# Kernel tuning notes

Measured on AMD Instinct MI355X. Metric: run time of the kernel, lower is better.

## Reference

```python
import jax, jax.numpy as jnp
import numpy as np

D_MODEL = 256
N_HEADS = 8
HEAD_DIM = D_MODEL // N_HEADS  # 32
N_LEVELS = 4
N_POINTS = 4
LEVEL_SHAPES = [(100, 100), (50, 50), (25, 25), (13, 13)]
LEVEL_STARTS = [0] + list(np.cumsum([h * w for h, w in LEVEL_SHAPES]))[:-1]
LEN_IN = int(sum(h * w for h, w in LEVEL_SHAPES))  # 13294
BATCH = 2
LEN_Q = LEN_IN  # encoder self-attention


def _offset_bias():
    # faithful to MSDeformAttn._reset_parameters for sampling_offsets bias
    thetas = np.arange(N_HEADS, dtype=np.float32) * (2.0 * np.pi / N_HEADS)
    grid = np.stack([np.cos(thetas), np.sin(thetas)], -1)
    grid = grid / np.abs(grid).max(-1, keepdims=True)
    grid = np.tile(grid.reshape(N_HEADS, 1, 1, 2), (1, N_LEVELS, N_POINTS, 1))
    for i in range(N_POINTS):
        grid[:, :, i, :] *= i + 1
    return jnp.asarray(grid.reshape(-1), dtype=jnp.float32)


def setup_inputs() -> dict:
    key = jax.random.key(0)
    ks = jax.random.split(key, 10)
    s = 1.0 / np.sqrt(D_MODEL)
    inp = {
        "query": jax.random.normal(ks[0], (BATCH, LEN_Q, D_MODEL), jnp.float32),
        "reference_points": jax.random.uniform(ks[1], (BATCH, LEN_Q, N_LEVELS, 2), jnp.float32),
        "input_flatten": jax.random.normal(ks[2], (BATCH, LEN_IN, D_MODEL), jnp.float32),
        "input_spatial_shapes": jnp.asarray(LEVEL_SHAPES, dtype=jnp.int32),
        "W_value": jax.random.normal(ks[3], (D_MODEL, D_MODEL), jnp.float32) * s,
        "b_value": jnp.zeros((D_MODEL,), jnp.float32),
        "W_off": jax.random.normal(ks[4], (D_MODEL, N_HEADS * N_LEVELS * N_POINTS * 2), jnp.float32) * 0.01,
        "b_off": _offset_bias(),
        "W_attn": jax.random.normal(ks[5], (D_MODEL, N_HEADS * N_LEVELS * N_POINTS), jnp.float32) * 0.01,
        "b_attn": jnp.zeros((N_HEADS * N_LEVELS * N_POINTS,), jnp.float32),
        "W_out": jax.random.normal(ks[6], (D_MODEL, D_MODEL), jnp.float32) * s,
        "b_out": jnp.zeros((D_MODEL,), jnp.float32),
    }
    return inp


def _corner(v_t, ix, iy, h, w):
    # v_t: (n, M, h*w, D); ix/iy: (n, M, LqP) int32. Zero padding outside.
    valid = (ix >= 0) & (ix < w) & (iy >= 0) & (iy < h)
    idx = jnp.clip(iy, 0, h - 1) * w + jnp.clip(ix, 0, w - 1)
    g = jnp.take_along_axis(v_t, idx[..., None], axis=2)  # (n, M, LqP, D)
    return g * valid[..., None].astype(v_t.dtype)


def _ms_deform_attn(query, reference_points, input_flatten,
                    W_value, b_value, W_off, b_off, W_attn, b_attn, W_out, b_out):
    n, lq, _ = query.shape
    value = (input_flatten @ W_value + b_value).reshape(n, LEN_IN, N_HEADS, HEAD_DIM)
    offs = (query @ W_off + b_off).reshape(n, lq, N_HEADS, N_LEVELS, N_POINTS, 2)
    aw = jax.nn.softmax(
        (query @ W_attn + b_attn).reshape(n, lq, N_HEADS, N_LEVELS * N_POINTS), axis=-1
    ).reshape(n, lq, N_HEADS, N_LEVELS, N_POINTS)
    # offset_normalizer = (w, h) per level
    norm = jnp.asarray([[w, h] for h, w in LEVEL_SHAPES], dtype=query.dtype)
    loc = reference_points[:, :, None, :, None, :] + offs / norm[None, None, None, :, None, :]

    acc = jnp.zeros((n, N_HEADS, lq, HEAD_DIM), dtype=value.dtype)
    for l, (h, w) in enumerate(LEVEL_SHAPES):
        s0 = LEVEL_STARTS[l]
        v_t = jnp.transpose(value[:, s0:s0 + h * w], (0, 2, 1, 3))  # (n, M, hw, D)
        ll = loc[:, :, :, l]  # (n, lq, M, P, 2) in [0,1]
        # grid_sample bilinear, align_corners=False: pixel = coord*size - 0.5
        x = ll[..., 0] * w - 0.5
        y = ll[..., 1] * h - 0.5
        x0 = jnp.floor(x); y0 = jnp.floor(y)
        tx = x - x0; ty = y - y0
        ix0 = x0.astype(jnp.int32); iy0 = y0.astype(jnp.int32)
        flat = lambda a: jnp.transpose(a, (0, 2, 1, 3)).reshape(n, N_HEADS, lq * N_POINTS)
        ix0f, iy0f = flat(ix0), flat(iy0)
        txf = flat(tx)[..., None]; tyf = flat(ty)[..., None]
        g00 = _corner(v_t, ix0f, iy0f, h, w)
        g01 = _corner(v_t, ix0f + 1, iy0f, h, w)
        g10 = _corner(v_t, ix0f, iy0f + 1, h, w)
        g11 = _corner(v_t, ix0f + 1, iy0f + 1, h, w)
        samp = (g00 * (1 - txf) * (1 - tyf) + g01 * txf * (1 - tyf)
                + g10 * (1 - txf) * tyf + g11 * txf * tyf)
        samp = samp.reshape(n, N_HEADS, lq, N_POINTS, HEAD_DIM)
        wl = jnp.transpose(aw[:, :, :, l], (0, 2, 1, 3))[..., None]  # (n, M, lq, P, 1)
        acc = acc + (samp * wl).sum(axis=3)

    out = jnp.transpose(acc, (0, 2, 1, 3)).reshape(n, lq, D_MODEL)
    return out @ W_out + b_out


def reference(query, reference_points, input_flatten, input_spatial_shapes,
              W_value, b_value, W_off, b_off, W_attn, b_attn, W_out, b_out):
    # input_spatial_shapes carried for signature fidelity; level geometry is static.
    return _ms_deform_attn(query, reference_points, input_flatten,
                           W_value, b_value, W_off, b_off, W_attn, b_attn, W_out, b_out)
```

## Files before the change

kernel.cpp:

```cpp
#include <hip/hip_runtime.h>

#define NH 8
#define HD 32
#define NL 4
#define NP 4
#define DM 256
#define LEN_IN_C 13294
#define LQ_C 13294
#define B_C 2
#define M_TOTAL (B_C * LQ_C)
#define MT_TILES 1662

typedef __attribute__((ext_vector_type(8))) short short8;
typedef __attribute__((ext_vector_type(4))) float floatx4;

__device__ __forceinline__ unsigned short f2bf(float x) {
    union { float f; unsigned int u; } a; a.f = x;
    unsigned int r = (a.u + 0x7FFFu + ((a.u >> 16) & 1u)) >> 16;
    return (unsigned short)r;
}
__device__ __forceinline__ float bflo(unsigned int u) {
    union { unsigned int u; float f; } a; a.u = u << 16; return a.f;
}
__device__ __forceinline__ float bfhi(unsigned int u) {
    union { unsigned int u; float f; } a; a.u = u & 0xffff0000u; return a.f;
}

__global__ __launch_bounds__(256) void conv_a_kernel(const float* __restrict__ A0,
                                                     unsigned short* __restrict__ D0,
                                                     const float* __restrict__ A1,
                                                     unsigned short* __restrict__ D1,
                                                     int M) {
    const float* A = blockIdx.y ? A1 : A0;
    unsigned short* Asw = blockIdx.y ? D1 : D0;
    const int u = blockIdx.x * 256 + threadIdx.x;
    const int lane = u & 63;
    const int kc = (u >> 6) & 7;
    const int rt = u >> 9;
    const int row = rt * 16 + (lane & 15);
    const int col0 = kc * 32 + (lane >> 4) * 8;
    unsigned short tmp[8];
    if (row < M) {
        const float4 f0 = *(const float4*)(A + (size_t)row * 256 + col0);
        const float4 f1 = *(const float4*)(A + (size_t)row * 256 + col0 + 4);
        tmp[0] = f2bf(f0.x); tmp[1] = f2bf(f0.y); tmp[2] = f2bf(f0.z); tmp[3] = f2bf(f0.w);
        tmp[4] = f2bf(f1.x); tmp[5] = f2bf(f1.y); tmp[6] = f2bf(f1.z); tmp[7] = f2bf(f1.w);
    } else {
#pragma unroll
        for (int j = 0; j < 8; ++j) tmp[j] = 0;
    }
    short8 v;
#pragma unroll
    for (int j = 0; j < 8; ++j) v[j] = (short)tmp[j];
    ((short8*)Asw)[u] = v;
}

__device__ __forceinline__ void conv_b_body(const float* __restrict__ W,
                                            unsigned short* __restrict__ Bsw,
                                            int Nsrc, int NTsrc, int NTtotal, int ntOff,
                                            int vblk) {
    const int u = vblk * 256 + threadIdx.x;
    const int lane = u & 63;
    const int unit = u >> 6;
    const int ntl = unit % NTsrc;
    const int kc = unit / NTsrc;
    const int n = ntl * 16 + (lane & 15);
    const int k0 = kc * 32 + (lane >> 4) * 8;
    short8 v;
#pragma unroll
    for (int j = 0; j < 8; ++j)
        v[j] = (short)f2bf(W[(size_t)(k0 + j) * Nsrc + n]);
    ((short8*)Bsw)[(size_t)(kc * NTtotal + ntOff + ntl) * 64 + lane] = v;
}

__global__ __launch_bounds__(256) void conv_weights_kernel(const float* __restrict__ Wv,
                                                           const float* __restrict__ Woff,
                                                           const float* __restrict__ Wattn,
                                                           const float* __restrict__ Wout,
                                                           const float* __restrict__ boff,
                                                           const float* __restrict__ battn,
                                                           unsigned short* __restrict__ BswV,
                                                           unsigned short* __restrict__ BswOA,
                                                           unsigned short* __restrict__ BswO,
                                                           float* __restrict__ fbias) {
    const int blk = blockIdx.x;
    if (blk < 32)        conv_b_body(Wv,    BswV,  256, 16, 16, 0,  blk);
    else if (blk < 64)   conv_b_body(Woff,  BswOA, 256, 16, 24, 0,  blk - 32);
    else if (blk < 80)   conv_b_body(Wattn, BswOA, 128,  8, 24, 16, blk - 64);
    else if (blk < 112)  conv_b_body(Wout,  BswO,  256, 16, 16, 0,  blk - 80);
    else {
        const int t = (blk - 112) * 256 + threadIdx.x;
        if (t < 384) fbias[t] = (t < 256) ? boff[t] : battn[t - 256];
    }
}

template <int NTW, bool OUT_BF16>
__device__ __forceinline__ void gemm_body_fk(const short8* __restrict__ Au,
                                             const short8* __restrict__ Bu,
                                             int ntBase, int NT_B,
                                             const float* __restrict__ bias,
                                             void* __restrict__ Cout, int Ncols,
                                             int M, int rt) {
    const int lane = threadIdx.x & 63;

    short8 a[8];
    short8 b[8][NTW];
#pragma unroll
    for (int kc = 0; kc < 8; ++kc) {
        a[kc] = Au[(size_t)(rt * 8 + kc) * 64 + lane];
#pragma unroll
        for (int t = 0; t < NTW; ++t)
            b[kc][t] = Bu[(size_t)(kc * NT_B + ntBase + t) * 64 + lane];
    }

    floatx4 acc[NTW];
#pragma unroll
    for (int t = 0; t < NTW; ++t) acc[t] = (floatx4){0.f, 0.f, 0.f, 0.f};

#pragma unroll
    for (int kc = 0; kc < 8; ++kc)
#pragma unroll
        for (int t = 0; t < NTW; ++t)
            acc[t] = __builtin_amdgcn_mfma_f32_16x16x32_bf16(a[kc], b[kc][t], acc[t], 0, 0, 0);

    const int colq = lane & 15;
    const int rowq = (lane >> 4) * 4;
#pragma unroll
    for (int t = 0; t < NTW; ++t) {
        const int col = (ntBase + t) * 16 + colq;
        const float bc = bias[col];
#pragma unroll
        for (int reg = 0; reg < 4; ++reg) {
            const int row = rt * 16 + rowq + reg;
            if (row < M) {
                const float v = acc[t][reg] + bc;
                if (OUT_BF16)
                    ((unsigned short*)Cout)[(size_t)row * Ncols + col] = f2bf(v);
                else
                    ((float*)Cout)[(size_t)row * Ncols + col] = v;
            }
        }
    }
}

__global__ __launch_bounds__(256, 2) void dual_gemm_kernel(const short8* __restrict__ AuV,
                                                           const short8* __restrict__ AuQ,
                                                           const short8* __restrict__ BuV,
                                                           const short8* __restrict__ BuOA,
                                                           const float* __restrict__ bv,
                                                           const float* __restrict__ fbias,
                                                           unsigned short* __restrict__ value,
                                                           float* __restrict__ fused, int M) {
    const int wave = (int)(threadIdx.x >> 6);
    const int bx = blockIdx.x;
    if (bx < MT_TILES)
        gemm_body_fk<4, true>(AuV, BuV, wave * 4, 16, bv, value, 256, M, bx);
    else if (bx < 2 * MT_TILES)
        gemm_body_fk<4, false>(AuQ, BuOA, wave * 4, 24, fbias, fused, 384, M, bx - MT_TILES);
    else
        gemm_body_fk<2, false>(AuQ, BuOA, 16 + wave * 2, 24, fbias, fused, 384, M, bx - 2 * MT_TILES);
}

__global__ __launch_bounds__(256, 2) void out_gemm_kernel(const short8* __restrict__ AuAcc,
                                                          const short8* __restrict__ BuO,
                                                          const float* __restrict__ bout,
                                                          float* __restrict__ out, int M) {
    const int wave = (int)(threadIdx.x >> 6);
    gemm_body_fk<4, false>(AuAcc, BuO, wave * 4, 16, bout, out, 256, M, blockIdx.x);
}

__global__ __launch_bounds__(256, 4) void msda_sample_kernel(const float* __restrict__ refp,
                                                             const unsigned short* __restrict__ value,
                                                             const float* __restrict__ fused,
                                                             unsigned short* __restrict__ AccSw) {
    constexpr int lvl_hw[4] = {100, 50, 25, 13};
    constexpr int lvl_s[4] = {0, 10000, 12500, 13125};

    const int bq0 = blockIdx.x * 4;
    const int tid = threadIdx.x;

    __shared__ float s_ref[32];
    __shared__ int4 s_pi[4 * 8 * 17];
    __shared__ float4 s_pw[4 * 8 * 17];

    if (tid < 32) s_ref[tid] = refp[(size_t)bq0 * 8 + tid];
    __syncthreads();

#pragma unroll
    for (int jj = 0; jj < 2; ++jj) {
        const int job = jj * 256 + tid;
        const int qq = job >> 7;
        const int t = job & 127;
        const int h = t >> 4;
        const int l = (t >> 2) & 3;
        const int bq = bq0 + qq;
        const int b = (bq >= LQ_C) ? 1 : 0;

        const float logit = fused[(size_t)bq * 384 + 256 + t];
        float mx = logit;
#pragma unroll
        for (int mask = 1; mask < 16; mask <<= 1) mx = fmaxf(mx, __shfl_xor(mx, mask));
        const float e = expf(logit - mx);
        float s = e;
#pragma unroll
        for (int mask = 1; mask < 16; mask <<= 1) s += __shfl_xor(s, mask);
        const float aw = e / s;

        const int whl = lvl_hw[l];
        const float fwh = (float)whl;
        const float2 oxy = *(const float2*)(fused + (size_t)bq * 384 + t * 2);
        const float x = s_ref[qq * 8 + l * 2] * fwh + oxy.x - 0.5f;
        const float y = s_ref[qq * 8 + l * 2 + 1] * fwh + oxy.y - 0.5f;
        const float x0f = floorf(x), y0f = floorf(y);
        const float tx = x - x0f, ty = y - y0f;
        const int ix0 = (int)x0f, iy0 = (int)y0f;

        const bool xv0 = (unsigned)ix0 < (unsigned)whl;
        const bool xv1 = (unsigned)(ix0 + 1) < (unsigned)whl;
        const bool yv0 = (unsigned)iy0 < (unsigned)whl;
        const bool yv1 = (unsigned)(iy0 + 1) < (unsigned)whl;

        const int cx0 = min(max(ix0, 0), whl - 1);
        const int cx1 = min(max(ix0 + 1, 0), whl - 1);
        const int cy0 = min(max(iy0, 0), whl - 1);
        const int cy1 = min(max(iy0 + 1, 0), whl - 1);

        const int base = (b * LEN_IN_C + lvl_s[l]) * 256 + h * 32;
        const int r0 = base + cy0 * (whl * 256);
        const int r1 = base + cy1 * (whl * 256);
        int4 ii;
        ii.x = (r0 + cx0 * 256) * 2;
        ii.y = (r0 + cx1 * 256) * 2;
        ii.z = (r1 + cx0 * 256) * 2;
        ii.w = (r1 + cx1 * 256) * 2;
        float4 wv;
        wv.x = (xv0 && yv0) ? aw * (1.f - tx) * (1.f - ty) : 0.f;
        wv.y = (xv1 && yv0) ? aw * tx * (1.f - ty) : 0.f;
        wv.z = (xv0 && yv1) ? aw * (1.f - tx) * ty : 0.f;
        wv.w = (xv1 && yv1) ? aw * tx * ty : 0.f;
        const int slot = (qq * 8 + h) * 17 + (t & 15);
        s_pi[slot] = ii;
        s_pw[slot] = wv;
    }
    __syncthreads();

    const int qq = tid >> 6;
    const int h = (tid >> 3) & 7;
    const int l8 = tid & 7;
    const char* vbp = (const char*)value + l8 * 8;
    const int pbase = (qq * 8 + h) * 17;

    float4 acc0 = {0.f, 0.f, 0.f, 0.f};
    float4 acc1 = {0.f, 0.f, 0.f, 0.f};
#pragma unroll
    for (int g = 0; g < 4; ++g) {
        int4 ii[4]; float4 ww[4]; uint2 v[16];
#pragma unroll
        for (int p = 0; p < 4; ++p) {
            ii[p] = s_pi[pbase + g * 4 + p];
            ww[p] = s_pw[pbase + g * 4 + p];
        }
#pragma unroll
        for (int p = 0; p < 4; ++p) {
            v[p * 4 + 0] = *(const uint2*)(vbp + ii[p].x);
            v[p * 4 + 1] = *(const uint2*)(vbp + ii[p].y);
            v[p * 4 + 2] = *(const uint2*)(vbp + ii[p].z);
            v[p * 4 + 3] = *(const uint2*)(vbp + ii[p].w);
        }
#pragma unroll
        for (int p = 0; p < 4; ++p) {
            const float4 wv = ww[p];
            const uint2 v00 = v[p * 4 + 0], v01 = v[p * 4 + 1];
            const uint2 v10 = v[p * 4 + 2], v11 = v[p * 4 + 3];
            acc0.x += wv.x * bflo(v00.x); acc0.y += wv.x * bfhi(v00.x);
            acc0.z += wv.x * bflo(v00.y); acc0.w += wv.x * bfhi(v00.y);
            acc1.x += wv.y * bflo(v01.x); acc1.y += wv.y * bfhi(v01.x);
            acc1.z += wv.y * bflo(v01.y); acc1.w += wv.y * bfhi(v01.y);
            acc0.x += wv.z * bflo(v10.x); acc0.y += wv.z * bfhi(v10.x);
            acc0.z += wv.z * bflo(v10.y); acc0.w += wv.z * bfhi(v10.y);
            acc1.x += wv.w * bflo(v11.x); acc1.y += wv.w * bfhi(v11.x);
            acc1.z += wv.w * bflo(v11.y); acc1.w += wv.w * bfhi(v11.y);
        }
    }
    const float4 acc = {acc0.x + acc1.x, acc0.y + acc1.y, acc0.z + acc1.z, acc0.w + acc1.w};

    const int bq = bq0 + qq;
    const int rt = bq >> 4, mm = bq & 15;
    const int col = h * 32 + l8 * 4;
    const int kc = col >> 5, q2 = (col >> 3) & 3, j = col & 7;
    unsigned int p0 = (unsigned int)f2bf(acc.x) | ((unsigned int)f2bf(acc.y) << 16);
    unsigned int p1 = (unsigned int)f2bf(acc.z) | ((unsigned int)f2bf(acc.w) << 16);
    uint2 pk; pk.x = p0; pk.y = p1;
    *(uint2*)(AccSw + ((size_t)((rt * 8 + kc) * 64 + (q2 * 16 + mm)) * 8 + j)) = pk;
}

extern "C" void kernel_launch(void* const* d_in, const int* in_sizes, int n_in,
                              void* d_out, int out_size, void* d_ws, size_t ws_size,
                              hipStream_t stream) {
    const float* query  = (const float*)d_in[0];
    const float* refp   = (const float*)d_in[1];
    const float* inflat = (const float*)d_in[2];
    const float* Wv    = (const float*)d_in[4];
    const float* bv    = (const float*)d_in[5];
    const float* Woff  = (const float*)d_in[6];
    const float* boff  = (const float*)d_in[7];
    const float* Wattn = (const float*)d_in[8];
    const float* battn = (const float*)d_in[9];
    const float* Wout  = (const float*)d_in[10];
    const float* bout  = (const float*)d_in[11];
    float* out = (float*)d_out;

    char* p = (char*)d_ws;
    const size_t aswBytes = (size_t)MT_TILES * 8 * 64 * 8 * sizeof(unsigned short);
    unsigned short* AswV = (unsigned short*)p;           p += aswBytes;
    unsigned short* AswQ = (unsigned short*)p;           p += aswBytes;
    unsigned short* BswV = (unsigned short*)p;           p += (size_t)8 * 16 * 64 * 8 * 2;
    unsigned short* BswOA = (unsigned short*)p;          p += (size_t)8 * 24 * 64 * 8 * 2;
    unsigned short* BswO = (unsigned short*)p;           p += (size_t)8 * 16 * 64 * 8 * 2;
    float* fbias = (float*)p;                            p += 384 * sizeof(float);
    unsigned short* value = (unsigned short*)p;          p += (size_t)M_TOTAL * 256 * 2;
    float* fused = (float*)p;                            p += (size_t)M_TOTAL * 384 * 4;
    unsigned short* AccSw = AswV;

    const int M = M_TOTAL;

    conv_weights_kernel<<<114, 256, 0, stream>>>(Wv, Woff, Wattn, Wout, boff, battn,
                                                 BswV, BswOA, BswO, fbias);
    conv_a_kernel<<<dim3(MT_TILES * 2, 2), 256, 0, stream>>>(inflat, AswV, query, AswQ, M);
    dual_gemm_kernel<<<MT_TILES * 3, 256, 0, stream>>>((const short8*)AswV, (const short8*)AswQ,
                                                       (const short8*)BswV, (const short8*)BswOA,
                                                       bv, fbias, value, fused, M);
    msda_sample_kernel<<<M / 4, 256, 0, stream>>>(refp, value, fused, AccSw);
    out_gemm_kernel<<<MT_TILES, 256, 0, stream>>>((const short8*)AccSw, (const short8*)BswO,
                                                  bout, out, M);
}
```

Measured before the change: 231.7 us.

## Stage GEMM tiles through LDS with async loads and 64x128 block tiles

Rewrites the projection and output GEMMs so each block computes a 64-row by 128-column tile. The A fragments are staged into LDS with global_load_lds, and B k-slices are double-buffered so the next slice loads while MFMAs run on the current one. The grid becomes 2D over row blocks and column groups, and the A workspace is padded to a multiple of 4 row tiles. The aim is to raise MFMA work per loaded byte and cut redundant B loads, at the cost of a barrier per k-step and more LDS use per block.

```diff
diff --git a/kernel.cpp b/kernel.cpp
--- a/kernel.cpp
+++ b/kernel.cpp
@@ -10,6 +10,8 @@
 #define B_C 2
 #define M_TOTAL (B_C * LQ_C)
 #define MT_TILES 1662
+#define MT_PAD 1664
+#define RBLK (MT_PAD / 4)
 
 typedef __attribute__((ext_vector_type(8))) short short8;
 typedef __attribute__((ext_vector_type(4))) float floatx4;
@@ -24,6 +26,12 @@
 }
 __device__ __forceinline__ float bfhi(unsigned int u) {
     union { unsigned int u; float f; } a; a.u = u & 0xffff0000u; return a.f;
+}
+
+__device__ __forceinline__ void glds16(const void* g, void* l) {
+    __builtin_amdgcn_global_load_lds(
+        (const __attribute__((address_space(1))) unsigned int*)g,
+        (__attribute__((address_space(3))) unsigned int*)l, 16, 0, 0);
 }
 
 __global__ __launch_bounds__(256) void conv_a_kernel(const float* __restrict__ A0,
@@ -94,56 +102,84 @@
     }
 }
 
-template <int NTW, bool OUT_BF16>
-__device__ __forceinline__ void gemm_body_fk(const short8* __restrict__ Au,
-                                             const short8* __restrict__ Bu,
-                                             int ntBase, int NT_B,
-                                             const float* __restrict__ bias,
-                                             void* __restrict__ Cout, int Ncols,
-                                             int M, int rt) {
-    const int lane = threadIdx.x & 63;
-
-    short8 a[8];
-    short8 b[8][NTW];
+template <bool OUT_BF16, int NT_B, int NCOLS>
+__device__ __forceinline__ void gemm_lds_body(short8* As, short8* Bs,
+                                              const short8* __restrict__ Au,
+                                              const short8* __restrict__ Bu,
+                                              int rtile0, int ntB,
+                                              const float* __restrict__ bias,
+                                              void* __restrict__ Cout, int M) {
+    const int tid = threadIdx.x;
+    const int lane = tid & 63;
+    const int wave = tid >> 6;
+
+#pragma unroll
+    for (int i = 0; i < 8; ++i)
+        glds16(&Au[(size_t)((rtile0 + wave) * 8 + i) * 64 + lane], &As[(wave * 8 + i) * 64]);
+#pragma unroll
+    for (int j = 0; j < 2; ++j) {
+        const int u = wave * 2 + j;
+        glds16(&Bu[(size_t)(ntB + u) * 64 + lane], &Bs[u * 64]);
+    }
+    __syncthreads();
+
+    floatx4 acc[4][2];
+#pragma unroll
+    for (int r = 0; r < 4; ++r)
+#pragma unroll
+        for (int j = 0; j < 2; ++j) acc[r][j] = (floatx4){0.f, 0.f, 0.f, 0.f};
+
 #pragma unroll
     for (int kc = 0; kc < 8; ++kc) {
-        a[kc] = Au[(size_t)(rt * 8 + kc) * 64 + lane];
-#pragma unroll
-        for (int t = 0; t < NTW; ++t)
-            b[kc][t] = Bu[(size_t)(kc * NT_B + ntBase + t) * 64 + lane];
-    }
-
-    floatx4 acc[NTW];
-#pragma unroll
-    for (int t = 0; t < NTW; ++t) acc[t] = (floatx4){0.f, 0.f, 0.f, 0.f};
-
-#pragma unroll
-    for (int kc = 0; kc < 8; ++kc)
-#pragma unroll
-        for (int t = 0; t < NTW; ++t)
-            acc[t] = __builtin_amdgcn_mfma_f32_16x16x32_bf16(a[kc], b[kc][t], acc[t], 0, 0, 0);
+        if (kc < 7) {
+#pragma unroll
+            for (int j = 0; j < 2; ++j) {
+                const int u = wave * 2 + j;
+                glds16(&Bu[(size_t)((kc + 1) * NT_B + ntB + u) * 64 + lane],
+                       &Bs[(((kc + 1) & 1) * 8 + u) * 64]);
+            }
+        }
+        const short8 a0 = As[(0 * 8 + kc) * 64 + lane];
+        const short8 a1 = As[(1 * 8 + kc) * 64 + lane];
+        const short8 a2 = As[(2 * 8 + kc) * 64 + lane];
+        const short8 a3 = As[(3 * 8 + kc) * 64 + lane];
+        const short8 b0 = Bs[((kc & 1) * 8 + wave * 2 + 0) * 64 + lane];
+        const short8 b1 = Bs[((kc & 1) * 8 + wave * 2 + 1) * 64 + lane];
+        acc[0][0] = __builtin_amdgcn_mfma_f32_16x16x32_bf16(a0, b0, acc[0][0], 0, 0, 0);
+        acc[0][1] = __builtin_amdgcn_mfma_f32_16x16x32_bf16(a0, b1, acc[0][1], 0, 0, 0);
+        acc[1][0] = __builtin_amdgcn_mfma_f32_16x16x32_bf16(a1, b0, acc[1][0], 0, 0, 0);
+        acc[1][1] = __builtin_amdgcn_mfma_f32_16x16x32_bf16(a1, b1, acc[1][1], 0, 0, 0);
+        acc[2][0] = __builtin_amdgcn_mfma_f32_16x16x32_bf16(a2, b0, acc[2][0], 0, 0, 0);
+        acc[2][1] = __builtin_amdgcn_mfma_f32_16x16x32_bf16(a2, b1, acc[2][1], 0, 0, 0);
+        acc[3][0] = __builtin_amdgcn_mfma_f32_16x16x32_bf16(a3, b0, acc[3][0], 0, 0, 0);
+        acc[3][1] = __builtin_amdgcn_mfma_f32_16x16x32_bf16(a3, b1, acc[3][1], 0, 0, 0);
+        __syncthreads();
+    }
 
     const int colq = lane & 15;
     const int rowq = (lane >> 4) * 4;
 #pragma unroll
-    for (int t = 0; t < NTW; ++t) {
-        const int col = (ntBase + t) * 16 + colq;
+    for (int j = 0; j < 2; ++j) {
+        const int col = (ntB + wave * 2 + j) * 16 + colq;
         const float bc = bias[col];
 #pragma unroll
-        for (int reg = 0; reg < 4; ++reg) {
-            const int row = rt * 16 + rowq + reg;
-            if (row < M) {
-                const float v = acc[t][reg] + bc;
-                if (OUT_BF16)
-                    ((unsigned short*)Cout)[(size_t)row * Ncols + col] = f2bf(v);
-                else
-                    ((float*)Cout)[(size_t)row * Ncols + col] = v;
+        for (int r = 0; r < 4; ++r) {
+#pragma unroll
+            for (int reg = 0; reg < 4; ++reg) {
+                const int row = (rtile0 + r) * 16 + rowq + reg;
+                if (row < M) {
+                    const float v = acc[r][j][reg] + bc;
+                    if (OUT_BF16)
+                        ((unsigned short*)Cout)[(size_t)row * NCOLS + col] = f2bf(v);
+                    else
+                        ((float*)Cout)[(size_t)row * NCOLS + col] = v;
+                }
             }
         }
     }
 }
 
-__global__ __launch_bounds__(256, 2) void dual_gemm_kernel(const short8* __restrict__ AuV,
+__global__ __launch_bounds__(256, 3) void dual_gemm_kernel(const short8* __restrict__ AuV,
                                                            const short8* __restrict__ AuQ,
                                                            const short8* __restrict__ BuV,
                                                            const short8* __restrict__ BuOA,
@@ -151,22 +187,24 @@
                                                            const float* __restrict__ fbias,
                                                            unsigned short* __restrict__ value,
                                                            float* __restrict__ fused, int M) {
-    const int wave = (int)(threadIdx.x >> 6);
-    const int bx = blockIdx.x;
-    if (bx < MT_TILES)
-        gemm_body_fk<4, true>(AuV, BuV, wave * 4, 16, bv, value, 256, M, bx);
-    else if (bx < 2 * MT_TILES)
-        gemm_body_fk<4, false>(AuQ, BuOA, wave * 4, 24, fbias, fused, 384, M, bx - MT_TILES);
+    __shared__ short8 As[32 * 64];
+    __shared__ short8 Bs[16 * 64];
+    const int rtile0 = blockIdx.x * 4;
+    const int y = blockIdx.y;
+    if (y < 2)
+        gemm_lds_body<true, 16, 256>(As, Bs, AuV, BuV, rtile0, y * 8, bv, value, M);
     else
-        gemm_body_fk<2, false>(AuQ, BuOA, 16 + wave * 2, 24, fbias, fused, 384, M, bx - 2 * MT_TILES);
-}
-
-__global__ __launch_bounds__(256, 2) void out_gemm_kernel(const short8* __restrict__ AuAcc,
+        gemm_lds_body<false, 24, 384>(As, Bs, AuQ, BuOA, rtile0, (y - 2) * 8, fbias, fused, M);
+}
+
+__global__ __launch_bounds__(256, 3) void out_gemm_kernel(const short8* __restrict__ AuAcc,
                                                           const short8* __restrict__ BuO,
                                                           const float* __restrict__ bout,
                                                           float* __restrict__ out, int M) {
-    const int wave = (int)(threadIdx.x >> 6);
-    gemm_body_fk<4, false>(AuAcc, BuO, wave * 4, 16, bout, out, 256, M, blockIdx.x);
+    __shared__ short8 As[32 * 64];
+    __shared__ short8 Bs[16 * 64];
+    gemm_lds_body<false, 16, 256>(As, Bs, AuAcc, BuO, blockIdx.x * 4, blockIdx.y * 8,
+                                  bout, out, M);
 }
 
 __global__ __launch_bounds__(256, 4) void msda_sample_kernel(const float* __restrict__ refp,
@@ -311,7 +349,7 @@
     float* out = (float*)d_out;
 
     char* p = (char*)d_ws;
-    const size_t aswBytes = (size_t)MT_TILES * 8 * 64 * 8 * sizeof(unsigned short);
+    const size_t aswBytes = (size_t)MT_PAD * 8 * 64 * 8 * sizeof(unsigned short);
     unsigned short* AswV = (unsigned short*)p;           p += aswBytes;
     unsigned short* AswQ = (unsigned short*)p;           p += aswBytes;
     unsigned short* BswV = (unsigned short*)p;           p += (size_t)8 * 16 * 64 * 8 * 2;
@@ -326,11 +364,11 @@
 
     conv_weights_kernel<<<114, 256, 0, stream>>>(Wv, Woff, Wattn, Wout, boff, battn,
                                                  BswV, BswOA, BswO, fbias);
-    conv_a_kernel<<<dim3(MT_TILES * 2, 2), 256, 0, stream>>>(inflat, AswV, query, AswQ, M);
-    dual_gemm_kernel<<<MT_TILES * 3, 256, 0, stream>>>((const short8*)AswV, (const short8*)AswQ,
-                                                       (const short8*)BswV, (const short8*)BswOA,
-                                                       bv, fbias, value, fused, M);
+    conv_a_kernel<<<dim3(MT_PAD * 2, 2), 256, 0, stream>>>(inflat, AswV, query, AswQ, M);
+    dual_gemm_kernel<<<dim3(RBLK, 5), 256, 0, stream>>>((const short8*)AswV, (const short8*)AswQ,
+                                                        (const short8*)BswV, (const short8*)BswOA,
+                                                        bv, fbias, value, fused, M);
     msda_sample_kernel<<<M / 4, 256, 0, stream>>>(refp, value, fused, AccSw);
-    out_gemm_kernel<<<MT_TILES, 256, 0, stream>>>((const short8*)AccSw, (const short8*)BswO,
-                                                  bout, out, M);
-}
+    out_gemm_kernel<<<dim3(RBLK, 2), 256, 0, stream>>>((const short8*)AccSw, (const short8*)BswO,
+                                                       bout, out, M);
+}
```

After: 231.1 us. About the same (-0.2%).
